# Kernel optimization log

Hardware: AMD Instinct MI355X
Metric: run time of the kernel (lower is better)

## Reference

```python
import jax, jax.numpy as jnp
import numpy as np

B, S, D, H = 4, 4096, 1024, 128

def setup_inputs() -> dict:
    key = jax.random.key(0)
    ks = jax.random.split(key, 4)
    scale = 1.0 / np.sqrt(D)
    return {
        "x":  jax.random.normal(ks[0], (B, S, D), dtype=jnp.float32),
        "Wq": jax.random.normal(ks[1], (D, H), dtype=jnp.float32) * scale,
        "bq": jnp.zeros((H,), dtype=jnp.float32),
        "Wk": jax.random.normal(ks[2], (D, H), dtype=jnp.float32) * scale,
        "bk": jnp.zeros((H,), dtype=jnp.float32),
        "Wv": jax.random.normal(ks[3], (D, H), dtype=jnp.float32) * scale,
        "bv": jnp.zeros((H,), dtype=jnp.float32),
    }

def reference(x, Wq, bq, Wk, bk, Wv, bv):
    # q, k, v: [B, S, H]
    q = x @ Wq + bq
    k = x @ Wk + bk
    v = x @ Wv + bv
    inv_sqrt_h = 1.0 / jnp.sqrt(jnp.asarray(q.shape[-1], q.dtype))
    # scores: [B, S, S]
    scores = jnp.einsum('bqh,bkh->bqk', q, k) * inv_sqrt_h
    seq = q.shape[1]
    causal = jnp.tril(jnp.ones((seq, seq), dtype=bool))
    scores = jnp.where(causal, scores, jnp.asarray(-jnp.inf, scores.dtype))
    probs = jax.nn.softmax(scores, axis=-1)
    # dropout p=0.0 -> identity
    return jnp.einsum('bqk,bkh->bqh', probs, v)
```

## Files before the change

kernel.cpp:

```cpp
#include <hip/hip_runtime.h>
#include <hip/hip_bf16.h>

#define B_ 4
#define S_ 4096
#define D_ 1024
#define H_ 128

typedef _Float16 half8 __attribute__((ext_vector_type(8)));
typedef _Float16 half4v __attribute__((ext_vector_type(4)));
typedef float float4v __attribute__((ext_vector_type(4)));


__global__ __launch_bounds__(256) void k_cvt_w(const float* __restrict__ Wq,
                                               const float* __restrict__ Wk,
                                               const float* __restrict__ Wv,
                                               _Float16* __restrict__ WT) {
    const float* W = blockIdx.y == 0 ? Wq : (blockIdx.y == 1 ? Wk : Wv);
    int idx = blockIdx.x * 256 + threadIdx.x;
    int k = idx >> 7, n = idx & 127;
    WT[(size_t)blockIdx.y * (H_ * D_) + (size_t)n * D_ + k] = (_Float16)W[idx];
}

__global__ __launch_bounds__(256, 3) void k_proj(const float* __restrict__ X,
                                                 const _Float16* __restrict__ WT,
                                                 const float* __restrict__ bq,
                                                 const float* __restrict__ bk,
                                                 const float* __restrict__ bv,
                                                 _Float16* __restrict__ Qf,
                                                 _Float16* __restrict__ Kz,
                                                 _Float16* __restrict__ Vz) {
    __shared__ _Float16 smem[64 * 136 + 128 * 136];
    _Float16* As = smem;
    _Float16* Bs = smem + 64 * 136;

    const int t    = threadIdx.x;
    const int bid  = blockIdx.x;
    const int w    = bid >> 8;
    const int m0   = (bid & 255) * 64;
    const int lane = t & 63, wid = t >> 6;
    const int lo   = lane & 15, hi = lane >> 4;
    const int wr   = wid >> 1, wc = wid & 1;

    const _Float16* Wt = WT + (size_t)w * (H_ * D_);

    const int xr = t >> 5, xc = (t & 31) * 4;
    const int br = t >> 4, bc = (t & 15) * 8;

    float4v xreg[8];
    half8   wreg[8];
#pragma unroll
    for (int i2 = 0; i2 < 8; ++i2)
        xreg[i2] = *(const float4v*)(X + (size_t)(m0 + xr + i2 * 8) * D_ + xc);
#pragma unroll
    for (int i2 = 0; i2 < 8; ++i2)
        wreg[i2] = *(const half8*)(Wt + (size_t)(br + i2 * 16) * D_ + bc);

    float4v acc[2][4];
#pragma unroll
    for (int mt = 0; mt < 2; ++mt)
#pragma unroll
        for (int nt = 0; nt < 4; ++nt) acc[mt][nt] = {0.f, 0.f, 0.f, 0.f};

    for (int it = 0; it < 8; ++it) {
        __syncthreads();
#pragma unroll
        for (int i2 = 0; i2 < 8; ++i2) {
            float4v xv = xreg[i2];
            half4v hv;
            hv[0] = (_Float16)xv[0]; hv[1] = (_Float16)xv[1];
            hv[2] = (_Float16)xv[2]; hv[3] = (_Float16)xv[3];
            *(half4v*)(&As[(xr + i2 * 8) * 136 + xc]) = hv;
        }
#pragma unroll
        for (int i2 = 0; i2 < 8; ++i2)
            *(half8*)(&Bs[(br + i2 * 16) * 136 + bc]) = wreg[i2];
        __syncthreads();
        if (it < 7) {
            const int k0n = (it + 1) * 128;
#pragma unroll
            for (int i2 = 0; i2 < 8; ++i2)
                xreg[i2] = *(const float4v*)(X + (size_t)(m0 + xr + i2 * 8) * D_ + k0n + xc);
#pragma unroll
            for (int i2 = 0; i2 < 8; ++i2)
                wreg[i2] = *(const half8*)(Wt + (size_t)(br + i2 * 16) * D_ + k0n + bc);
        }
#pragma unroll
        for (int kk = 0; kk < 4; ++kk) {
            half8 af[2], bf[4];
#pragma unroll
            for (int mt = 0; mt < 2; ++mt)
                af[mt] = *(const half8*)(&As[(wr * 32 + mt * 16 + lo) * 136 + kk * 32 + hi * 8]);
#pragma unroll
            for (int nt = 0; nt < 4; ++nt)
                bf[nt] = *(const half8*)(&Bs[(wc * 64 + nt * 16 + lo) * 136 + kk * 32 + hi * 8]);
#pragma unroll
            for (int mt = 0; mt < 2; ++mt)
#pragma unroll
                for (int nt = 0; nt < 4; ++nt)
                    acc[mt][nt] = __builtin_amdgcn_mfma_f32_16x16x32_f16(
                        af[mt], bf[nt], acc[mt][nt], 0, 0, 0);
        }
    }

    const float* bias = (w == 0) ? bq : ((w == 1) ? bk : bv);
    const float scale = (w == 0) ? (0.08838834764831845f * 1.4426950408889634f) : 1.0f;
    __syncthreads();
    _Float16* Ct = smem;
#pragma unroll
    for (int mt = 0; mt < 2; ++mt)
#pragma unroll
        for (int nt = 0; nt < 4; ++nt) {
            const int col   = wc * 64 + nt * 16 + lo;
            const float bn  = bias[col];
            const int rbase = wr * 32 + mt * 16 + 4 * hi;
#pragma unroll
            for (int j = 0; j < 4; ++j)
                Ct[(rbase + j) * 136 + col] = (_Float16)((acc[mt][nt][j] + bn) * scale);
        }
    __syncthreads();

    const int bb  = m0 >> 12;
    const int tt0 = (m0 & (S_ - 1)) >> 5;

    if (w == 0) {
        const int r = t >> 2, c0 = (t & 3) * 32;
        _Float16* dst = Qf + (size_t)(m0 + r) * H_ + c0;
        const _Float16* srcp = &Ct[r * 136 + c0];
#pragma unroll
        for (int cc = 0; cc < 4; ++cc)
            *(half8*)(dst + cc * 8) = *(const half8*)(srcp + cc * 8);
    } else if (w == 1) {
        const int rowp = ((lo >> 2) << 3) + (lo & 3);
#pragma unroll
        for (int q = 0; q < 4; ++q) {
            const int fid = wid * 4 + q;
            const int ft = fid >> 3, k2 = (fid >> 1) & 3, c = fid & 1;
            const int row = ft * 32 + rowp + 4 * c;
            half8 v = *(const half8*)(&Ct[row * 136 + k2 * 32 + hi * 8]);
            *(half8*)(Kz + (size_t)(bb * 128 + tt0 + ft) * 4096 +
                      (k2 * 2 + c) * 512 + lane * 8) = v;
        }
    } else {
#pragma unroll
        for (int q = 0; q < 4; ++q) {
            const int fid = wid * 4 + q;
            const int ft = fid >> 3, hc = fid & 7;
            half8 v;
#pragma unroll
            for (int e = 0; e < 8; ++e)
                v[e] = Ct[(ft * 32 + hi * 8 + e) * 136 + hc * 16 + lo];
            *(half8*)(Vz + (size_t)(bb * 128 + tt0 + ft) * 4096 +
                      hc * 512 + lane * 8) = v;
        }
    }
}

__global__ __launch_bounds__(512, 2) void k_attn(const _Float16* __restrict__ Qf,
                                                 const _Float16* __restrict__ Kz,
                                                 const _Float16* __restrict__ Vz,
                                                 float* __restrict__ Out) {
    __shared__ float    sm_l[8][32];
    __shared__ _Float16 sm_o[8][32][136];

    const int t    = threadIdx.x;
    const int lane = t & 63, wid = t >> 6;
    const int lo = lane & 15, hi = lane >> 4;

    const int i   = blockIdx.x;
    const int b   = (i >> 1) & 3;
    const int qtr = ((i >> 3) << 1) | (i & 1);
    const int qt  = (qtr < 64) ? qtr : (191 - qtr);
    const int q0  = qt << 5;

    const _Float16* Qb = Qf + (size_t)b * (S_ * H_);
    const _Float16* Kb = Kz + (size_t)b * 524288;
    const _Float16* Vb = Vz + (size_t)b * 524288;

    half8 qfa[4], qfb[4];
#pragma unroll
    for (int kk = 0; kk < 4; ++kk) {
        qfa[kk] = *(const half8*)(Qb + (size_t)(q0 + lo) * H_ + kk * 32 + hi * 8);
        qfb[kk] = *(const half8*)(Qb + (size_t)(q0 + 16 + lo) * H_ + kk * 32 + hi * 8);
    }

    float4v oa[8], ob[8];
#pragma unroll
    for (int hc = 0; hc < 8; ++hc) { oa[hc] = {0.f,0.f,0.f,0.f}; ob[hc] = {0.f,0.f,0.f,0.f}; }
    float la = 0.f, lb = 0.f;

    const int lane8 = lane * 8;
    const int ntiles = qt + 1;

    half8 kc0[4], kc1[4];
    if (wid < ntiles) {
        const _Float16* Kt = Kb + (size_t)wid * 4096 + lane8;
#pragma unroll
        for (int kk = 0; kk < 4; ++kk) {
            kc0[kk] = *(const half8*)(Kt + (kk * 2    ) * 512);
            kc1[kk] = *(const half8*)(Kt + (kk * 2 + 1) * 512);
        }
    }

    for (int tt = wid; tt < ntiles; tt += 8) {
        const _Float16* Vt = Vb + (size_t)tt * 4096 + lane8;
        half8 vf[8];
#pragma unroll
        for (int hc = 0; hc < 8; ++hc)
            vf[hc] = *(const half8*)(Vt + hc * 512);
        const int tn = (tt + 8 < ntiles) ? (tt + 8) : tt;
        half8 kn0[4], kn1[4];
        {
            const _Float16* Ktn = Kb + (size_t)tn * 4096 + lane8;
#pragma unroll
            for (int kk = 0; kk < 4; ++kk) {
                kn0[kk] = *(const half8*)(Ktn + (kk * 2    ) * 512);
                kn1[kk] = *(const half8*)(Ktn + (kk * 2 + 1) * 512);
            }
        }
        float4v s0a = {0.f,0.f,0.f,0.f}, s1a = {0.f,0.f,0.f,0.f};
        float4v s0b = {0.f,0.f,0.f,0.f}, s1b = {0.f,0.f,0.f,0.f};
#pragma unroll
        for (int kk = 0; kk < 4; ++kk) {
            s0a = __builtin_amdgcn_mfma_f32_16x16x32_f16(kc0[kk], qfa[kk], s0a, 0, 0, 0);
            s0b = __builtin_amdgcn_mfma_f32_16x16x32_f16(kc0[kk], qfb[kk], s0b, 0, 0, 0);
            s1a = __builtin_amdgcn_mfma_f32_16x16x32_f16(kc1[kk], qfa[kk], s1a, 0, 0, 0);
            s1b = __builtin_amdgcn_mfma_f32_16x16x32_f16(kc1[kk], qfb[kk], s1b, 0, 0, 0);
        }
        if (tt == qt) {
#pragma unroll
            for (int j = 0; j < 4; ++j) {
                const int c0 = 8 * hi + j, c1 = 8 * hi + 4 + j;
                if (c0 > lo)      s0a[j] = -INFINITY;
                if (c1 > lo)      s1a[j] = -INFINITY;
                if (c0 > 16 + lo) s0b[j] = -INFINITY;
                if (c1 > 16 + lo) s1b[j] = -INFINITY;
            }
        }
        float pa0 = __builtin_amdgcn_exp2f(s0a[0]), pa1 = __builtin_amdgcn_exp2f(s0a[1]);
        float pa2 = __builtin_amdgcn_exp2f(s0a[2]), pa3 = __builtin_amdgcn_exp2f(s0a[3]);
        float pa4 = __builtin_amdgcn_exp2f(s1a[0]), pa5 = __builtin_amdgcn_exp2f(s1a[1]);
        float pa6 = __builtin_amdgcn_exp2f(s1a[2]), pa7 = __builtin_amdgcn_exp2f(s1a[3]);
        float pb0 = __builtin_amdgcn_exp2f(s0b[0]), pb1 = __builtin_amdgcn_exp2f(s0b[1]);
        float pb2 = __builtin_amdgcn_exp2f(s0b[2]), pb3 = __builtin_amdgcn_exp2f(s0b[3]);
        float pb4 = __builtin_amdgcn_exp2f(s1b[0]), pb5 = __builtin_amdgcn_exp2f(s1b[1]);
        float pb6 = __builtin_amdgcn_exp2f(s1b[2]), pb7 = __builtin_amdgcn_exp2f(s1b[3]);
        la += ((pa0+pa1)+(pa2+pa3)) + ((pa4+pa5)+(pa6+pa7));
        lb += ((pb0+pb1)+(pb2+pb3)) + ((pb4+pb5)+(pb6+pb7));
        half8 pfa, pfb;
        pfa[0]=(_Float16)pa0; pfa[1]=(_Float16)pa1; pfa[2]=(_Float16)pa2; pfa[3]=(_Float16)pa3;
        pfa[4]=(_Float16)pa4; pfa[5]=(_Float16)pa5; pfa[6]=(_Float16)pa6; pfa[7]=(_Float16)pa7;
        pfb[0]=(_Float16)pb0; pfb[1]=(_Float16)pb1; pfb[2]=(_Float16)pb2; pfb[3]=(_Float16)pb3;
        pfb[4]=(_Float16)pb4; pfb[5]=(_Float16)pb5; pfb[6]=(_Float16)pb6; pfb[7]=(_Float16)pb7;
#pragma unroll
        for (int hc = 0; hc < 8; ++hc) {
            oa[hc] = __builtin_amdgcn_mfma_f32_16x16x32_f16(vf[hc], pfa, oa[hc], 0, 0, 0);
            ob[hc] = __builtin_amdgcn_mfma_f32_16x16x32_f16(vf[hc], pfb, ob[hc], 0, 0, 0);
        }
#pragma unroll
        for (int kk = 0; kk < 4; ++kk) { kc0[kk] = kn0[kk]; kc1[kk] = kn1[kk]; }
    }

    la += __shfl_xor(la, 16); la += __shfl_xor(la, 32);
    lb += __shfl_xor(lb, 16); lb += __shfl_xor(lb, 32);

    sm_l[wid][lo]      = la;
    sm_l[wid][16 + lo] = lb;
#pragma unroll
    for (int hc = 0; hc < 8; ++hc) {
        half4v va, vb;
#pragma unroll
        for (int j = 0; j < 4; ++j) { va[j] = (_Float16)oa[hc][j]; vb[j] = (_Float16)ob[hc][j]; }
        *(half4v*)(&sm_o[wid][lo][hc * 16 + 4 * hi])      = va;
        *(half4v*)(&sm_o[wid][16 + lo][hc * 16 + 4 * hi]) = vb;
    }
    __syncthreads();

#pragma unroll
    for (int qh = 0; qh < 2; ++qh) {
        const int q = qh * 16 + lo;
        float L = 0.f;
#pragma unroll
        for (int w = 0; w < 8; ++w) L += sm_l[w][q];
        const float invL = 1.f / L;
        float4v ov = {0.f, 0.f, 0.f, 0.f};
#pragma unroll
        for (int w = 0; w < 8; ++w) {
            half4v tv = *(const half4v*)(&sm_o[w][q][wid * 16 + 4 * hi]);
#pragma unroll
            for (int j = 0; j < 4; ++j) ov[j] += (float)tv[j];
        }
#pragma unroll
        for (int j = 0; j < 4; ++j) ov[j] *= invL;
        *(float4v*)(Out + ((size_t)b * S_ + q0 + q) * H_ + wid * 16 + 4 * hi) = ov;
    }
}

extern "C" void kernel_launch(void* const* d_in, const int* in_sizes, int n_in,
                              void* d_out, int out_size, void* d_ws, size_t ws_size,
                              hipStream_t stream) {
    const float* x  = (const float*)d_in[0];
    const float* Wq = (const float*)d_in[1];
    const float* bq = (const float*)d_in[2];
    const float* Wk = (const float*)d_in[3];
    const float* bk = (const float*)d_in[4];
    const float* Wv = (const float*)d_in[5];
    const float* bv = (const float*)d_in[6];
    float* out = (float*)d_out;

    char* ws = (char*)d_ws;
    _Float16* WT = (_Float16*)ws;
    _Float16* Qf = (_Float16*)(ws + 786432);
    _Float16* Kz = (_Float16*)(ws + 786432 + 4194304);
    _Float16* Vz = (_Float16*)(ws + 786432 + 8388608);

    hipLaunchKernelGGL(k_cvt_w, dim3(512, 3), dim3(256), 0, stream, Wq, Wk, Wv, WT);
    hipLaunchKernelGGL(k_proj, dim3(768), dim3(256), 0, stream,
                       x, WT, bq, bk, bv, Qf, Kz, Vz);
    hipLaunchKernelGGL(k_attn, dim3(512), dim3(512), 0, stream, Qf, Kz, Vz, out);
}
```

Measured before the change: 65.47 us.

## Pre-swizzle weights into MFMA fragment layout and load B directly from global

Result: slower. 76.74 us (+17.2%).

```diff
diff --git a/kernel.cpp b/kernel.cpp
--- a/kernel.cpp
+++ b/kernel.cpp
@@ -14,24 +14,27 @@
 __global__ __launch_bounds__(256) void k_cvt_w(const float* __restrict__ Wq,
                                                const float* __restrict__ Wk,
                                                const float* __restrict__ Wv,
-                                               _Float16* __restrict__ WT) {
+                                               _Float16* __restrict__ WTz) {
     const float* W = blockIdx.y == 0 ? Wq : (blockIdx.y == 1 ? Wk : Wv);
-    int idx = blockIdx.x * 256 + threadIdx.x;
-    int k = idx >> 7, n = idx & 127;
-    WT[(size_t)blockIdx.y * (H_ * D_) + (size_t)n * D_ + k] = (_Float16)W[idx];
+    const int idx  = blockIdx.x * 256 + threadIdx.x;
+    const int lane = idx & 63, nt = (idx >> 6) & 7, K32 = idx >> 9;
+    const int lo = lane & 15, hi = lane >> 4;
+    half8 v;
+#pragma unroll
+    for (int e = 0; e < 8; ++e)
+        v[e] = (_Float16)W[(K32 * 32 + hi * 8 + e) * H_ + nt * 16 + lo];
+    *(half8*)(WTz + (size_t)(((int)blockIdx.y * 32 + K32) * 8 + nt) * 512 + lane * 8) = v;
 }
 
 __global__ __launch_bounds__(256, 3) void k_proj(const float* __restrict__ X,
-                                                 const _Float16* __restrict__ WT,
+                                                 const _Float16* __restrict__ WTz,
                                                  const float* __restrict__ bq,
                                                  const float* __restrict__ bk,
                                                  const float* __restrict__ bv,
                                                  _Float16* __restrict__ Qf,
                                                  _Float16* __restrict__ Kz,
                                                  _Float16* __restrict__ Vz) {
-    __shared__ _Float16 smem[64 * 136 + 128 * 136];
-    _Float16* As = smem;
-    _Float16* Bs = smem + 64 * 136;
+    __shared__ _Float16 smem[64 * 136];
 
     const int t    = threadIdx.x;
     const int bid  = blockIdx.x;
@@ -39,84 +42,62 @@
     const int m0   = (bid & 255) * 64;
     const int lane = t & 63, wid = t >> 6;
     const int lo   = lane & 15, hi = lane >> 4;
-    const int wr   = wid >> 1, wc = wid & 1;
-
-    const _Float16* Wt = WT + (size_t)w * (H_ * D_);
-
-    const int xr = t >> 5, xc = (t & 31) * 4;
-    const int br = t >> 4, bc = (t & 15) * 8;
+
+    _Float16* Aw = smem + wid * (16 * 136);
+    const float* Xw = X + (size_t)(m0 + wid * 16) * D_;
+    const _Float16* Wz = WTz + (size_t)(w * 32 * 8) * 512 + lane * 8;
+
+    const int sr = lane >> 5, sc = (lane & 31) * 4;
 
     float4v xreg[8];
-    half8   wreg[8];
 #pragma unroll
     for (int i2 = 0; i2 < 8; ++i2)
-        xreg[i2] = *(const float4v*)(X + (size_t)(m0 + xr + i2 * 8) * D_ + xc);
-#pragma unroll
-    for (int i2 = 0; i2 < 8; ++i2)
-        wreg[i2] = *(const half8*)(Wt + (size_t)(br + i2 * 16) * D_ + bc);
-
-    float4v acc[2][4];
-#pragma unroll
-    for (int mt = 0; mt < 2; ++mt)
-#pragma unroll
-        for (int nt = 0; nt < 4; ++nt) acc[mt][nt] = {0.f, 0.f, 0.f, 0.f};
+        xreg[i2] = *(const float4v*)(Xw + (size_t)(i2 * 2 + sr) * D_ + sc);
+
+    float4v acc[8];
+#pragma unroll
+    for (int nt = 0; nt < 8; ++nt) acc[nt] = {0.f, 0.f, 0.f, 0.f};
 
     for (int it = 0; it < 8; ++it) {
-        __syncthreads();
 #pragma unroll
         for (int i2 = 0; i2 < 8; ++i2) {
             float4v xv = xreg[i2];
             half4v hv;
             hv[0] = (_Float16)xv[0]; hv[1] = (_Float16)xv[1];
             hv[2] = (_Float16)xv[2]; hv[3] = (_Float16)xv[3];
-            *(half4v*)(&As[(xr + i2 * 8) * 136 + xc]) = hv;
-        }
-#pragma unroll
-        for (int i2 = 0; i2 < 8; ++i2)
-            *(half8*)(&Bs[(br + i2 * 16) * 136 + bc]) = wreg[i2];
-        __syncthreads();
+            *(half4v*)(&Aw[(i2 * 2 + sr) * 136 + sc]) = hv;
+        }
         if (it < 7) {
             const int k0n = (it + 1) * 128;
 #pragma unroll
             for (int i2 = 0; i2 < 8; ++i2)
-                xreg[i2] = *(const float4v*)(X + (size_t)(m0 + xr + i2 * 8) * D_ + k0n + xc);
-#pragma unroll
-            for (int i2 = 0; i2 < 8; ++i2)
-                wreg[i2] = *(const half8*)(Wt + (size_t)(br + i2 * 16) * D_ + k0n + bc);
-        }
-#pragma unroll
-        for (int kk = 0; kk < 4; ++kk) {
-            half8 af[2], bf[4];
-#pragma unroll
-            for (int mt = 0; mt < 2; ++mt)
-                af[mt] = *(const half8*)(&As[(wr * 32 + mt * 16 + lo) * 136 + kk * 32 + hi * 8]);
-#pragma unroll
-            for (int nt = 0; nt < 4; ++nt)
-                bf[nt] = *(const half8*)(&Bs[(wc * 64 + nt * 16 + lo) * 136 + kk * 32 + hi * 8]);
-#pragma unroll
-            for (int mt = 0; mt < 2; ++mt)
-#pragma unroll
-                for (int nt = 0; nt < 4; ++nt)
-                    acc[mt][nt] = __builtin_amdgcn_mfma_f32_16x16x32_f16(
-                        af[mt], bf[nt], acc[mt][nt], 0, 0, 0);
+                xreg[i2] = *(const float4v*)(Xw + (size_t)(i2 * 2 + sr) * D_ + k0n + sc);
+        }
+#pragma unroll
+        for (int k32 = 0; k32 < 4; ++k32) {
+            const int K32 = it * 4 + k32;
+            half8 af = *(const half8*)(&Aw[lo * 136 + k32 * 32 + hi * 8]);
+            const _Float16* bp = Wz + (size_t)(K32 * 8) * 512;
+#pragma unroll
+            for (int nt = 0; nt < 8; ++nt) {
+                half8 bf = *(const half8*)(bp + (size_t)nt * 512);
+                acc[nt] = __builtin_amdgcn_mfma_f32_16x16x32_f16(af, bf, acc[nt], 0, 0, 0);
+            }
         }
     }
 
     const float* bias = (w == 0) ? bq : ((w == 1) ? bk : bv);
     const float scale = (w == 0) ? (0.08838834764831845f * 1.4426950408889634f) : 1.0f;
-    __syncthreads();
     _Float16* Ct = smem;
 #pragma unroll
-    for (int mt = 0; mt < 2; ++mt)
-#pragma unroll
-        for (int nt = 0; nt < 4; ++nt) {
-            const int col   = wc * 64 + nt * 16 + lo;
-            const float bn  = bias[col];
-            const int rbase = wr * 32 + mt * 16 + 4 * hi;
-#pragma unroll
-            for (int j = 0; j < 4; ++j)
-                Ct[(rbase + j) * 136 + col] = (_Float16)((acc[mt][nt][j] + bn) * scale);
-        }
+    for (int nt = 0; nt < 8; ++nt) {
+        const int col  = nt * 16 + lo;
+        const float bn = bias[col];
+#pragma unroll
+        for (int j = 0; j < 4; ++j)
+            Ct[(wid * 16 + 4 * hi + j) * 136 + col] =
+                (_Float16)((acc[nt][j] + bn) * scale);
+    }
     __syncthreads();
 
     const int bb  = m0 >> 12;
@@ -308,13 +289,13 @@
     float* out = (float*)d_out;
 
     char* ws = (char*)d_ws;
-    _Float16* WT = (_Float16*)ws;
-    _Float16* Qf = (_Float16*)(ws + 786432);
-    _Float16* Kz = (_Float16*)(ws + 786432 + 4194304);
-    _Float16* Vz = (_Float16*)(ws + 786432 + 8388608);
-
-    hipLaunchKernelGGL(k_cvt_w, dim3(512, 3), dim3(256), 0, stream, Wq, Wk, Wv, WT);
+    _Float16* WTz = (_Float16*)ws;
+    _Float16* Qf  = (_Float16*)(ws + 786432);
+    _Float16* Kz  = (_Float16*)(ws + 786432 + 4194304);
+    _Float16* Vz  = (_Float16*)(ws + 786432 + 8388608);
+
+    hipLaunchKernelGGL(k_cvt_w, dim3(64, 3), dim3(256), 0, stream, Wq, Wk, Wv, WTz);
     hipLaunchKernelGGL(k_proj, dim3(768), dim3(256), 0, stream,
-                       x, WT, bq, bk, bv, Qf, Kz, Vz);
+                       x, WTz, bq, bk, bv, Qf, Kz, Vz);
     hipLaunchKernelGGL(k_attn, dim3(512), dim3(512), 0, stream, Qf, Kz, Vz, out);
 }
```
